# Optimization experiments

Hardware: AMD Instinct MI355X
Metric: run time of the kernel (lower is better)

## Reference

```python
import jax, jax.numpy as jnp
import numpy as np

D_MODEL = 1024
D_OUT = 128  # output_embed_size (head dim)

def setup_inputs() -> dict:
    key = jax.random.key(0)
    ks = jax.random.split(key, 4)
    x = jax.random.normal(ks[0], (2, 4096, D_MODEL), dtype=jnp.float32)
    # weights mimic nn.init.normal_(std=0.02), biases zero
    qW_w = 0.02 * jax.random.normal(ks[1], (D_OUT, D_MODEL), dtype=jnp.float32)
    kW_w = 0.02 * jax.random.normal(ks[2], (D_OUT, D_MODEL), dtype=jnp.float32)
    vW_w = 0.02 * jax.random.normal(ks[3], (D_OUT, D_MODEL), dtype=jnp.float32)
    zb = jnp.zeros((D_OUT,), dtype=jnp.float32)
    return {"x": x, "qW_w": qW_w, "qW_b": zb, "kW_w": kW_w, "kW_b": zb,
            "vW_w": vW_w, "vW_b": zb}

def reference(x, qW_w, qW_b, kW_w, kW_b, vW_w, vW_b):
    # Linear: y = x @ W^T + b
    Q = jnp.einsum('bsd,ed->bse', x, qW_w) + qW_b  # [B,S,E]
    K = jnp.einsum('bsd,ed->bse', x, kW_w) + kW_b
    V = jnp.einsum('bsd,ed->bse', x, vW_w) + vW_b
    scale = 1.0 / jnp.sqrt(jnp.float32(D_OUT))
    attention = jnp.einsum('bqe,bke->bqk', Q, K) * scale  # [B,S,S], NO softmax
    output = jnp.einsum('bqk,bke->bqe', attention, V)     # [B,S,E]
    return output
```

## Files before the change

### kernel.cpp

```cpp
#include <hip/hip_runtime.h>

#define SS 4096
#define DD 1024
#define EE 128
#define SCALE 0.08838834764831845f

typedef __bf16 bf16x8 __attribute__((ext_vector_type(8)));
typedef float  f32x4  __attribute__((ext_vector_type(4)));

__device__ __forceinline__ void gload16(const void* g, void* l) {
  __builtin_amdgcn_global_load_lds(
      (const __attribute__((address_space(1))) void*)g,
      (__attribute__((address_space(3))) void*)l, 16, 0, 0);
}

__global__ __launch_bounds__(256, 3) void proj_kernel(
    const float* __restrict__ x,
    const float* __restrict__ qW, const float* __restrict__ qB,
    const float* __restrict__ kW, const float* __restrict__ kB,
    const float* __restrict__ vW, const float* __restrict__ vB,
    __bf16* __restrict__ Qbf, __bf16* __restrict__ KT, __bf16* __restrict__ VT)
{
  __shared__ __attribute__((aligned(16))) float  ldsA[2][64 * 64];
  __shared__ __attribute__((aligned(16))) __bf16 ldsB[2][64 * 64];

  const int tid  = threadIdx.x;
  const int w    = tid >> 6, lane = tid & 63;
  const int l15  = lane & 15, l4 = lane >> 4;
  const int wr   = w >> 1, wc = w & 1;

  const int id   = blockIdx.x;
  const int swz  = (id & 7) * 96 + (id >> 3);
  const int rt   = swz / 6, ct = swz % 6;
  const int row0 = rt * 64;
  const int g0   = ct * 64;

  const float* __restrict__ Wsel = (ct < 2) ? qW : (ct < 4 ? kW : vW);
  const float* __restrict__ bias = (ct < 2) ? qB : (ct < 4 ? kB : vB);
  const int bofs = (ct < 2) ? g0 : (ct < 4 ? g0 - 128 : g0 - 256);

  const int aRow = lane >> 4;
  const int aPos = lane & 15;
  const int cE   = aPos ^ aRow;
  const int cO   = aPos ^ (4 | aRow);
  const float* gAe = x + (size_t)(row0 + w * 16 + aRow) * DD + cE * 4;
  const float* gAo = x + (size_t)(row0 + w * 16 + aRow) * DD + cO * 4;

  const int brow = tid >> 2;
  const int bseg = tid & 3;
  const int brs  = brow & 7;
  const float* gBW = Wsel + (size_t)(bofs + brow) * DD + bseg * 16;

  f32x4 acc[2][2] = {};
  f32x4 rB[4];

#define BLOAD(T) {                                                           \
    const float* g_ = gBW + (T) * 64;                                        \
    rB[0] = *(const f32x4*)(g_);      rB[1] = *(const f32x4*)(g_ + 4);       \
    rB[2] = *(const f32x4*)(g_ + 8);  rB[3] = *(const f32x4*)(g_ + 12); }

#define BWRITE(P) {                                                          \
    bf16x8 v0_ = { (__bf16)rB[0][0], (__bf16)rB[0][1], (__bf16)rB[0][2],     \
                   (__bf16)rB[0][3], (__bf16)rB[1][0], (__bf16)rB[1][1],     \
                   (__bf16)rB[1][2], (__bf16)rB[1][3] };                     \
    bf16x8 v1_ = { (__bf16)rB[2][0], (__bf16)rB[2][1], (__bf16)rB[2][2],     \
                   (__bf16)rB[2][3], (__bf16)rB[3][0], (__bf16)rB[3][1],     \
                   (__bf16)rB[3][2], (__bf16)rB[3][3] };                     \
    *(bf16x8*)&ldsB[P][brow * 64 + (((bseg * 2)     ^ brs) << 3)] = v0_;     \
    *(bf16x8*)&ldsB[P][brow * 64 + (((bseg * 2 + 1) ^ brs) << 3)] = v1_; }

#define ASTAGE(P, T) {                                                       \
    const int k0_ = (T) * 64;                                                \
    gload16(gAe + k0_,                    &ldsA[P][(w * 16 +  0) * 64]);     \
    gload16(gAo + k0_ + (size_t) 4 * DD,  &ldsA[P][(w * 16 +  4) * 64]);     \
    gload16(gAe + k0_ + (size_t) 8 * DD,  &ldsA[P][(w * 16 +  8) * 64]);     \
    gload16(gAo + k0_ + (size_t)12 * DD,  &ldsA[P][(w * 16 + 12) * 64]);     }

#define CVT8(LO, HI) (bf16x8){ (__bf16)(LO)[0], (__bf16)(LO)[1],             \
    (__bf16)(LO)[2], (__bf16)(LO)[3], (__bf16)(HI)[0], (__bf16)(HI)[1],      \
    (__bf16)(HI)[2], (__bf16)(HI)[3] }

#define COMPUTE(P) {                                                         \
    const int rs7 = l15 & 7;                                                 \
    _Pragma("unroll") for (int ks = 0; ks < 2; ++ks) {                       \
      bf16x8 af[2], bq[2];                                                   \
      _Pragma("unroll") for (int m = 0; m < 2; ++m) {                        \
        const int row = wr * 32 + m * 16 + l15;                              \
        const int c0 = ks * 8 + l4 * 2;                                      \
        f32x4 lo = *(const f32x4*)&ldsA[P][row * 64 + (( c0      ^ rs7) << 2)]; \
        f32x4 hi = *(const f32x4*)&ldsA[P][row * 64 + (((c0 + 1) ^ rs7) << 2)]; \
        af[m] = CVT8(lo, hi);                                                \
      }                                                                      \
      _Pragma("unroll") for (int n = 0; n < 2; ++n) {                        \
        const int row = wc * 32 + n * 16 + l15;                              \
        bq[n] = *(const bf16x8*)&ldsB[P][row * 64 + (((ks*4 + l4) ^ rs7) << 3)]; \
      }                                                                      \
      acc[0][0] = __builtin_amdgcn_mfma_f32_16x16x32_bf16(af[0],bq[0],acc[0][0],0,0,0); \
      acc[0][1] = __builtin_amdgcn_mfma_f32_16x16x32_bf16(af[0],bq[1],acc[0][1],0,0,0); \
      acc[1][0] = __builtin_amdgcn_mfma_f32_16x16x32_bf16(af[1],bq[0],acc[1][0],0,0,0); \
      acc[1][1] = __builtin_amdgcn_mfma_f32_16x16x32_bf16(af[1],bq[1],acc[1][1],0,0,0); \
    } }

  BLOAD(0);
  ASTAGE(0, 0);
  BWRITE(0);
  __syncthreads();
  for (int t = 0; t < 15; ++t) {
    const int P = t & 1;
    BLOAD(t + 1);
    ASTAGE(P ^ 1, t + 1);
    COMPUTE(P);
    BWRITE(P ^ 1);
    __syncthreads();
  }
  COMPUTE(1);
  __syncthreads();
#undef BLOAD
#undef BWRITE
#undef ASTAGE
#undef CVT8
#undef COMPUTE

  if (ct < 2) {
    #pragma unroll
    for (int m = 0; m < 2; ++m)
      #pragma unroll
      for (int n = 0; n < 2; ++n) {
        const int col = wc * 32 + n * 16 + l15;
        const float bv = bias[bofs + col];
        #pragma unroll
        for (int r = 0; r < 4; ++r) {
          const int row = row0 + wr * 32 + m * 16 + l4 * 4 + r;
          Qbf[(size_t)row * EE + g0 + col] =
              (__bf16)((acc[m][n][r] + bv) * SCALE);
        }
      }
  } else {
    __bf16* Tb = (__bf16*)ldsA;
    #pragma unroll
    for (int m = 0; m < 2; ++m)
      #pragma unroll
      for (int n = 0; n < 2; ++n) {
        const int tc = wc * 32 + n * 16 + l15;
        const float bv = bias[bofs + tc];
        #pragma unroll
        for (int r = 0; r < 4; ++r) {
          const int rl = wr * 32 + m * 16 + l4 * 4 + r;
          Tb[tc * 64 + (((rl >> 3) ^ (tc & 7)) << 3) + (rl & 7)] =
              (__bf16)(acc[m][n][r] + bv);
        }
      }
    __syncthreads();
    const int col = tid >> 2, p2 = tid & 3;
    const int b = row0 >> 12, s0 = row0 & 4095;
    __bf16* dst = (ct < 4)
        ? &KT[((size_t)b * EE + (ct - 2) * 64 + col) * SS + s0]
        : &VT[((size_t)b * EE + (ct - 4) * 64 + col) * SS + s0];
    #pragma unroll
    for (int j = 0; j < 2; ++j) {
      const int ch = p2 * 2 + j;
      bf16x8 v = *(const bf16x8*)&Tb[col * 64 + ((ch ^ (col & 7)) << 3)];
      *(bf16x8*)&dst[ch * 8] = v;
    }
  }
}

__global__ __launch_bounds__(256) void ktv_kernel(
    const __bf16* __restrict__ KT, const __bf16* __restrict__ VT,
    float* __restrict__ part)
{
  const int c = blockIdx.x, fh = blockIdx.y, b = blockIdx.z;
  const int tid = threadIdx.x;
  const int w = tid >> 6, lane = tid & 63;
  const int l15 = lane & 15, l4 = lane >> 4;
  const int s0 = c * 64;
  const int fbase = fh * 64 + w * 16;
  const __bf16* Kb = KT + (size_t)b * EE * SS;
  const __bf16* Vb = VT + (size_t)b * EE * SS;

  f32x4 acc[8] = {};
  #pragma unroll
  for (int ks = 0; ks < 2; ++ks) {
    const int s = s0 + ks * 32 + 8 * l4;
    bf16x8 bv = *(const bf16x8*)&Vb[(size_t)(fbase + l15) * SS + s];
    #pragma unroll
    for (int i = 0; i < 8; ++i) {
      bf16x8 av = *(const bf16x8*)&Kb[(size_t)(i * 16 + l15) * SS + s];
      acc[i] = __builtin_amdgcn_mfma_f32_16x16x32_bf16(av, bv, acc[i], 0, 0, 0);
    }
  }
  float* P = part + (size_t)(b * 64 + c) * 16384;
  #pragma unroll
  for (int i = 0; i < 8; ++i)
    #pragma unroll
    for (int r = 0; r < 4; ++r) {
      int e = i * 16 + l4 * 4 + r;
      int f = fbase + l15;
      P[e * 128 + f] = acc[i][r];
    }
}

__global__ __launch_bounds__(256) void reduce_kernel(
    const float* __restrict__ part, __bf16* __restrict__ MT)
{
  const int b = blockIdx.y;
  const int e = blockIdx.x * 2 + (threadIdx.x >> 7);
  const int f = threadIdx.x & 127;
  float s = 0.f;
  for (int cc = 0; cc < 64; ++cc)
    s += part[(size_t)(b * 64 + cc) * 16384 + e * 128 + f];
  MT[((size_t)b * EE + f) * EE + e] = (__bf16)s;
}

__global__ __launch_bounds__(128) void qm_kernel(
    const __bf16* __restrict__ Qbf, const __bf16* __restrict__ MT,
    float* __restrict__ out)
{
  const int b = blockIdx.y;
  const int tid = threadIdx.x;
  const int w = tid >> 6, lane = tid & 63;
  const int l15 = lane & 15, l4 = lane >> 4;
  const int row0 = blockIdx.x * 32 + w * 16;
  const __bf16* Qb = Qbf + (size_t)b * SS * EE;
  const __bf16* Mb = MT + (size_t)b * EE * EE;

  f32x4 acc[8] = {};
  #pragma unroll
  for (int ks = 0; ks < 4; ++ks) {
    const int e = ks * 32 + 8 * l4;
    bf16x8 av = *(const bf16x8*)&Qb[(size_t)(row0 + l15) * EE + e];
    #pragma unroll
    for (int j = 0; j < 8; ++j) {
      bf16x8 bv = *(const bf16x8*)&Mb[(size_t)(j * 16 + l15) * EE + e];
      acc[j] = __builtin_amdgcn_mfma_f32_16x16x32_bf16(av, bv, acc[j], 0, 0, 0);
    }
  }
  #pragma unroll
  for (int j = 0; j < 8; ++j)
    #pragma unroll
    for (int r = 0; r < 4; ++r) {
      int srow = row0 + l4 * 4 + r;
      int f = j * 16 + l15;
      out[((size_t)b * SS + srow) * EE + f] = acc[j][r];
    }
}

extern "C" void kernel_launch(void* const* d_in, const int* in_sizes, int n_in,
                              void* d_out, int out_size, void* d_ws, size_t ws_size,
                              hipStream_t stream) {
  const float* x  = (const float*)d_in[0];
  const float* qW = (const float*)d_in[1];
  const float* qB = (const float*)d_in[2];
  const float* kW = (const float*)d_in[3];
  const float* kB = (const float*)d_in[4];
  const float* vW = (const float*)d_in[5];
  const float* vB = (const float*)d_in[6];
  float* out = (float*)d_out;

  char* base = (char*)d_ws;
  __bf16* Qbf = (__bf16*)(base);
  __bf16* KT  = (__bf16*)(base + (2u  << 20));
  __bf16* VT  = (__bf16*)(base + (4u  << 20));
  float*  part= (float*) (base + (6u  << 20));
  __bf16* MT  = (__bf16*)(base + (14u << 20));

  proj_kernel  <<<dim3(768),      256, 0, stream>>>(x, qW, qB, kW, kB, vW, vB,
                                                    Qbf, KT, VT);
  ktv_kernel   <<<dim3(64, 2, 2), 256, 0, stream>>>(KT, VT, part);
  reduce_kernel<<<dim3(64, 2),    256, 0, stream>>>(part, MT);
  qm_kernel    <<<dim3(128, 2),   128, 0, stream>>>(Qbf, MT, out);
}
```

Measured before the change: 43.22 us.

## Enlarge projection tiles to 128x128 and stage bf16 x through registers

The projection GEMM moves from 64x64 tiles (768 blocks) to 128x128 tiles (192 blocks), so each wave computes a 4x4 grid of MFMA tiles and x is re-read from global memory fewer times across output columns. x is no longer copied into LDS as fp32 by direct global-to-LDS loads. It is now loaded into registers, converted to bf16 once and stored into LDS, which halves the LDS footprint per element and removes the repeated conversion inside the compute loop. The cost is more registers, fewer blocks than the 256 CUs (under one wave of blocks) and loss of asynchronous global-to-LDS loads, so latency hiding may suffer.

Measured after the change: 69.55 us. 1.61x slower.

```diff
diff --git a/kernel.cpp b/kernel.cpp
--- a/kernel.cpp
+++ b/kernel.cpp
@@ -8,21 +8,15 @@
 typedef __bf16 bf16x8 __attribute__((ext_vector_type(8)));
 typedef float  f32x4  __attribute__((ext_vector_type(4)));
 
-__device__ __forceinline__ void gload16(const void* g, void* l) {
-  __builtin_amdgcn_global_load_lds(
-      (const __attribute__((address_space(1))) void*)g,
-      (__attribute__((address_space(3))) void*)l, 16, 0, 0);
-}
-
-__global__ __launch_bounds__(256, 3) void proj_kernel(
+__global__ __launch_bounds__(256) void proj_kernel(
     const float* __restrict__ x,
     const float* __restrict__ qW, const float* __restrict__ qB,
     const float* __restrict__ kW, const float* __restrict__ kB,
     const float* __restrict__ vW, const float* __restrict__ vB,
     __bf16* __restrict__ Qbf, __bf16* __restrict__ KT, __bf16* __restrict__ VT)
 {
-  __shared__ __attribute__((aligned(16))) float  ldsA[2][64 * 64];
-  __shared__ __attribute__((aligned(16))) __bf16 ldsB[2][64 * 64];
+  __shared__ __attribute__((aligned(16))) __bf16 ldsA[2][128 * 64];
+  __shared__ __attribute__((aligned(16))) __bf16 ldsB[2][128 * 64];
 
   const int tid  = threadIdx.x;
   const int w    = tid >> 6, lane = tid & 63;
@@ -30,136 +24,111 @@
   const int wr   = w >> 1, wc = w & 1;
 
   const int id   = blockIdx.x;
-  const int swz  = (id & 7) * 96 + (id >> 3);
-  const int rt   = swz / 6, ct = swz % 6;
-  const int row0 = rt * 64;
-  const int g0   = ct * 64;
-
-  const float* __restrict__ Wsel = (ct < 2) ? qW : (ct < 4 ? kW : vW);
-  const float* __restrict__ bias = (ct < 2) ? qB : (ct < 4 ? kB : vB);
-  const int bofs = (ct < 2) ? g0 : (ct < 4 ? g0 - 128 : g0 - 256);
-
-  const int aRow = lane >> 4;
-  const int aPos = lane & 15;
-  const int cE   = aPos ^ aRow;
-  const int cO   = aPos ^ (4 | aRow);
-  const float* gAe = x + (size_t)(row0 + w * 16 + aRow) * DD + cE * 4;
-  const float* gAo = x + (size_t)(row0 + w * 16 + aRow) * DD + cO * 4;
-
-  const int brow = tid >> 2;
-  const int bseg = tid & 3;
-  const int brs  = brow & 7;
-  const float* gBW = Wsel + (size_t)(bofs + brow) * DD + bseg * 16;
-
-  f32x4 acc[2][2] = {};
-  f32x4 rB[4];
-
-#define BLOAD(T) {                                                           \
-    const float* g_ = gBW + (T) * 64;                                        \
-    rB[0] = *(const f32x4*)(g_);      rB[1] = *(const f32x4*)(g_ + 4);       \
-    rB[2] = *(const f32x4*)(g_ + 8);  rB[3] = *(const f32x4*)(g_ + 12); }
-
-#define BWRITE(P) {                                                          \
-    bf16x8 v0_ = { (__bf16)rB[0][0], (__bf16)rB[0][1], (__bf16)rB[0][2],     \
-                   (__bf16)rB[0][3], (__bf16)rB[1][0], (__bf16)rB[1][1],     \
-                   (__bf16)rB[1][2], (__bf16)rB[1][3] };                     \
-    bf16x8 v1_ = { (__bf16)rB[2][0], (__bf16)rB[2][1], (__bf16)rB[2][2],     \
-                   (__bf16)rB[2][3], (__bf16)rB[3][0], (__bf16)rB[3][1],     \
-                   (__bf16)rB[3][2], (__bf16)rB[3][3] };                     \
-    *(bf16x8*)&ldsB[P][brow * 64 + (((bseg * 2)     ^ brs) << 3)] = v0_;     \
-    *(bf16x8*)&ldsB[P][brow * 64 + (((bseg * 2 + 1) ^ brs) << 3)] = v1_; }
-
-#define ASTAGE(P, T) {                                                       \
-    const int k0_ = (T) * 64;                                                \
-    gload16(gAe + k0_,                    &ldsA[P][(w * 16 +  0) * 64]);     \
-    gload16(gAo + k0_ + (size_t) 4 * DD,  &ldsA[P][(w * 16 +  4) * 64]);     \
-    gload16(gAe + k0_ + (size_t) 8 * DD,  &ldsA[P][(w * 16 +  8) * 64]);     \
-    gload16(gAo + k0_ + (size_t)12 * DD,  &ldsA[P][(w * 16 + 12) * 64]);     }
-
-#define CVT8(LO, HI) (bf16x8){ (__bf16)(LO)[0], (__bf16)(LO)[1],             \
-    (__bf16)(LO)[2], (__bf16)(LO)[3], (__bf16)(HI)[0], (__bf16)(HI)[1],      \
-    (__bf16)(HI)[2], (__bf16)(HI)[3] }
+  const int swz  = (id & 7) * 24 + (id >> 3);
+  const int rt   = swz / 3, ct = swz % 3;
+  const int row0 = rt * 128;
+
+  const float* __restrict__ Wsel = (ct == 0) ? qW : (ct == 1 ? kW : vW);
+  const float* __restrict__ bias = (ct == 0) ? qB : (ct == 1 ? kB : vB);
+
+  const int srow = tid >> 1;
+  const int sseg = tid & 1;
+  const int srs  = srow & 7;
+  const float* gA = x    + (size_t)(row0 + srow) * DD + sseg * 32;
+  const float* gB = Wsel + (size_t)srow * DD + sseg * 32;
+
+  f32x4 acc[4][4] = {};
+  f32x4 rA[8], rB[8];
+
+#define LOADS(T) {                                                           \
+    const float* ga_ = gA + (T) * 64;                                        \
+    const float* gb_ = gB + (T) * 64;                                        \
+    _Pragma("unroll") for (int q = 0; q < 8; ++q) {                          \
+      rA[q] = *(const f32x4*)(ga_ + q * 4);                                  \
+      rB[q] = *(const f32x4*)(gb_ + q * 4);                                  \
+    } }
+
+#define WRITES(P) {                                                          \
+    _Pragma("unroll") for (int qq = 0; qq < 4; ++qq) {                       \
+      bf16x8 va_ = { (__bf16)rA[2*qq][0], (__bf16)rA[2*qq][1],               \
+                     (__bf16)rA[2*qq][2], (__bf16)rA[2*qq][3],               \
+                     (__bf16)rA[2*qq+1][0], (__bf16)rA[2*qq+1][1],           \
+                     (__bf16)rA[2*qq+1][2], (__bf16)rA[2*qq+1][3] };         \
+      bf16x8 vb_ = { (__bf16)rB[2*qq][0], (__bf16)rB[2*qq][1],               \
+                     (__bf16)rB[2*qq][2], (__bf16)rB[2*qq][3],               \
+                     (__bf16)rB[2*qq+1][0], (__bf16)rB[2*qq+1][1],           \
+                     (__bf16)rB[2*qq+1][2], (__bf16)rB[2*qq+1][3] };         \
+      const int ch_ = (sseg * 4 + qq) ^ srs;                                 \
+      *(bf16x8*)&ldsA[P][srow * 64 + (ch_ << 3)] = va_;                      \
+      *(bf16x8*)&ldsB[P][srow * 64 + (ch_ << 3)] = vb_;                      \
+    } }
 
 #define COMPUTE(P) {                                                         \
     const int rs7 = l15 & 7;                                                 \
     _Pragma("unroll") for (int ks = 0; ks < 2; ++ks) {                       \
-      bf16x8 af[2], bq[2];                                                   \
-      _Pragma("unroll") for (int m = 0; m < 2; ++m) {                        \
-        const int row = wr * 32 + m * 16 + l15;                              \
-        const int c0 = ks * 8 + l4 * 2;                                      \
-        f32x4 lo = *(const f32x4*)&ldsA[P][row * 64 + (( c0      ^ rs7) << 2)]; \
-        f32x4 hi = *(const f32x4*)&ldsA[P][row * 64 + (((c0 + 1) ^ rs7) << 2)]; \
-        af[m] = CVT8(lo, hi);                                                \
-      }                                                                      \
-      _Pragma("unroll") for (int n = 0; n < 2; ++n) {                        \
-        const int row = wc * 32 + n * 16 + l15;                              \
-        bq[n] = *(const bf16x8*)&ldsB[P][row * 64 + (((ks*4 + l4) ^ rs7) << 3)]; \
-      }                                                                      \
-      acc[0][0] = __builtin_amdgcn_mfma_f32_16x16x32_bf16(af[0],bq[0],acc[0][0],0,0,0); \
-      acc[0][1] = __builtin_amdgcn_mfma_f32_16x16x32_bf16(af[0],bq[1],acc[0][1],0,0,0); \
-      acc[1][0] = __builtin_amdgcn_mfma_f32_16x16x32_bf16(af[1],bq[0],acc[1][0],0,0,0); \
-      acc[1][1] = __builtin_amdgcn_mfma_f32_16x16x32_bf16(af[1],bq[1],acc[1][1],0,0,0); \
+      const int so = ((ks * 4 + l4) ^ rs7) << 3;                             \
+      bf16x8 af[4], bq[4];                                                   \
+      _Pragma("unroll") for (int m = 0; m < 4; ++m)                          \
+        af[m] = *(const bf16x8*)&ldsA[P][(wr * 64 + m * 16 + l15) * 64 + so];\
+      _Pragma("unroll") for (int n = 0; n < 4; ++n)                          \
+        bq[n] = *(const bf16x8*)&ldsB[P][(wc * 64 + n * 16 + l15) * 64 + so];\
+      _Pragma("unroll") for (int m = 0; m < 4; ++m)                          \
+        _Pragma("unroll") for (int n = 0; n < 4; ++n)                        \
+          acc[m][n] = __builtin_amdgcn_mfma_f32_16x16x32_bf16(               \
+              af[m], bq[n], acc[m][n], 0, 0, 0);                             \
     } }
 
-  BLOAD(0);
-  ASTAGE(0, 0);
-  BWRITE(0);
+  LOADS(0);
+  WRITES(0);
   __syncthreads();
-  for (int t = 0; t < 15; ++t) {
+  for (int t = 0; t < 16; ++t) {
     const int P = t & 1;
-    BLOAD(t + 1);
-    ASTAGE(P ^ 1, t + 1);
+    if (t < 15) LOADS(t + 1);
     COMPUTE(P);
-    BWRITE(P ^ 1);
+    if (t < 15) WRITES(P ^ 1);
     __syncthreads();
   }
-  COMPUTE(1);
-  __syncthreads();
-#undef BLOAD
-#undef BWRITE
-#undef ASTAGE
-#undef CVT8
+#undef LOADS
+#undef WRITES
 #undef COMPUTE
 
-  if (ct < 2) {
-    #pragma unroll
-    for (int m = 0; m < 2; ++m)
+  if (ct == 0) {
+    #pragma unroll
+    for (int m = 0; m < 4; ++m)
       #pragma unroll
-      for (int n = 0; n < 2; ++n) {
-        const int col = wc * 32 + n * 16 + l15;
-        const float bv = bias[bofs + col];
+      for (int n = 0; n < 4; ++n) {
+        const int col = wc * 64 + n * 16 + l15;
+        const float bv = bias[col];
         #pragma unroll
         for (int r = 0; r < 4; ++r) {
-          const int row = row0 + wr * 32 + m * 16 + l4 * 4 + r;
-          Qbf[(size_t)row * EE + g0 + col] =
+          const int row = row0 + wr * 64 + m * 16 + l4 * 4 + r;
+          Qbf[(size_t)row * EE + col] =
               (__bf16)((acc[m][n][r] + bv) * SCALE);
         }
       }
   } else {
     __bf16* Tb = (__bf16*)ldsA;
     #pragma unroll
-    for (int m = 0; m < 2; ++m)
+    for (int m = 0; m < 4; ++m)
       #pragma unroll
-      for (int n = 0; n < 2; ++n) {
-        const int tc = wc * 32 + n * 16 + l15;
-        const float bv = bias[bofs + tc];
+      for (int n = 0; n < 4; ++n) {
+        const int tc = wc * 64 + n * 16 + l15;
+        const float bv = bias[tc];
         #pragma unroll
         for (int r = 0; r < 4; ++r) {
-          const int rl = wr * 32 + m * 16 + l4 * 4 + r;
-          Tb[tc * 64 + (((rl >> 3) ^ (tc & 7)) << 3) + (rl & 7)] =
+          const int rl = wr * 64 + m * 16 + l4 * 4 + r;
+          Tb[tc * 128 + (((rl >> 3) ^ (tc & 7)) << 3) + (rl & 7)] =
               (__bf16)(acc[m][n][r] + bv);
         }
       }
     __syncthreads();
-    const int col = tid >> 2, p2 = tid & 3;
+    const int col = tid >> 1, p2 = tid & 1;
     const int b = row0 >> 12, s0 = row0 & 4095;
-    __bf16* dst = (ct < 4)
-        ? &KT[((size_t)b * EE + (ct - 2) * 64 + col) * SS + s0]
-        : &VT[((size_t)b * EE + (ct - 4) * 64 + col) * SS + s0];
-    #pragma unroll
-    for (int j = 0; j < 2; ++j) {
-      const int ch = p2 * 2 + j;
-      bf16x8 v = *(const bf16x8*)&Tb[col * 64 + ((ch ^ (col & 7)) << 3)];
+    __bf16* dst = ((ct == 1) ? KT : VT) + ((size_t)b * EE + col) * SS + s0;
+    #pragma unroll
+    for (int j = 0; j < 8; ++j) {
+      const int ch = p2 * 8 + j;
+      bf16x8 v = *(const bf16x8*)&Tb[col * 128 + ((ch ^ (col & 7)) << 3)];
       *(bf16x8*)&dst[ch * 8] = v;
     }
   }
@@ -264,7 +233,7 @@
   float*  part= (float*) (base + (6u  << 20));
   __bf16* MT  = (__bf16*)(base + (14u << 20));
 
-  proj_kernel  <<<dim3(768),      256, 0, stream>>>(x, qW, qB, kW, kB, vW, vB,
+  proj_kernel  <<<dim3(192),      256, 0, stream>>>(x, qW, qB, kW, kB, vW, vB,
                                                     Qbf, KT, VT);
   ktv_kernel   <<<dim3(64, 2, 2), 256, 0, stream>>>(KT, VT, part);
   reduce_kernel<<<dim3(64, 2),    256, 0, stream>>>(part, MT);
```
